# Kernel optimization log

Hardware: AMD Instinct MI355X
Metric: run time of the kernel (lower is better)

## Reference

```python
import jax, jax.numpy as jnp
import numpy as np

B, S, H = 4, 2048, 16
HID = 2048
Q_LORA = 1536
KV_LORA = 512
D_NOPE, D_ROPE, D_V = 128, 64, 128
D_QK = D_NOPE + D_ROPE  # 192
THETA = 10000.0
EPS = 1e-6


def rms_norm(x, w):
    var = jnp.mean(jnp.square(x), axis=-1, keepdims=True)
    return x * jax.lax.rsqrt(var + EPS) * w


def rotate_half(x):
    x1, x2 = jnp.split(x, 2, axis=-1)
    return jnp.concatenate([-x2, x1], axis=-1)


def apply_rope(x, cos, sin):
    # DeepSeek de-interleaves pairs before the rotate_half formulation
    b, h, s, d = x.shape
    x = x.reshape(b, h, s, d // 2, 2).transpose(0, 1, 2, 4, 3).reshape(b, h, s, d)
    return x * cos + rotate_half(x) * sin


def setup_inputs() -> dict:
    key = jax.random.key(0)
    ks = jax.random.split(key, 8)
    sc = lambda fan_in: 1.0 / np.sqrt(fan_in)
    return {
        "x": jax.random.normal(ks[0], (B, S, HID), jnp.float32),
        "q_a_w": jax.random.normal(ks[1], (Q_LORA, HID), jnp.float32) * sc(HID),
        "q_a_ln_w": jnp.ones((Q_LORA,), jnp.float32),
        "q_b_w": jax.random.normal(ks[2], (H * D_QK, Q_LORA), jnp.float32) * sc(Q_LORA),
        "kv_a_w": jax.random.normal(ks[3], (KV_LORA + D_ROPE, HID), jnp.float32) * sc(HID),
        "kv_a_ln_w": jnp.ones((KV_LORA,), jnp.float32),
        "kv_b_w": jax.random.normal(ks[4], (H * (D_NOPE + D_V), KV_LORA), jnp.float32) * sc(KV_LORA),
        "o_w": jax.random.normal(ks[5], (HID, H * D_V), jnp.float32) * sc(H * D_V),
    }


def reference(x, q_a_w, q_a_ln_w, q_b_w, kv_a_w, kv_a_ln_w, kv_b_w, o_w):
    b, s, _ = x.shape
    # --- Q path: low-rank down-proj -> RMSNorm -> up-proj ---
    q = rms_norm(x @ q_a_w.T, q_a_ln_w) @ q_b_w.T          # [b,s,H*D_QK]
    q = q.reshape(b, s, H, D_QK).transpose(0, 2, 1, 3)      # [b,H,s,D_QK]
    q_nope, q_pe = q[..., :D_NOPE], q[..., D_NOPE:]
    # --- KV path: joint low-rank compression + shared rope key ---
    ckv = x @ kv_a_w.T                                      # [b,s,KV_LORA+D_ROPE]
    c_kv, k_pe = ckv[..., :KV_LORA], ckv[..., KV_LORA:]
    k_pe = k_pe.reshape(b, 1, s, D_ROPE)                    # shared across heads (MQA-style)
    kv = rms_norm(c_kv, kv_a_ln_w) @ kv_b_w.T               # [b,s,H*(D_NOPE+D_V)]
    kv = kv.reshape(b, s, H, D_NOPE + D_V).transpose(0, 2, 1, 3)
    k_nope, v = kv[..., :D_NOPE], kv[..., D_NOPE:]
    # --- decoupled RoPE on the rope sub-dims ---
    inv_freq = 1.0 / (THETA ** (jnp.arange(0, D_ROPE, 2, dtype=jnp.float32) / D_ROPE))
    t = jnp.arange(s, dtype=jnp.float32)
    emb = jnp.concatenate([jnp.outer(t, inv_freq)] * 2, axis=-1)  # [s,D_ROPE]
    cos, sin = jnp.cos(emb)[None, None], jnp.sin(emb)[None, None]
    q_pe = apply_rope(q_pe, cos, sin)
    k_pe = apply_rope(k_pe, cos, sin)
    # --- attention (wrapper's all-True mask => unmasked softmax) ---
    q_full = jnp.concatenate([q_nope, q_pe], axis=-1)                       # [b,H,s,192]
    k_full = jnp.concatenate([k_nope, jnp.broadcast_to(k_pe, (b, H, s, D_ROPE))], axis=-1)
    scale = D_QK ** -0.5
    scores = jnp.einsum('bhqd,bhkd->bhqk', q_full, k_full) * scale
    attn = jax.nn.softmax(scores, axis=-1)
    out = jnp.einsum('bhqk,bhkd->bhqd', attn, v)
    out = out.transpose(0, 2, 1, 3).reshape(b, s, H * D_V)
    return out @ o_w.T
```

## Files before the change

kernel.cpp:

```cpp
#include <hip/hip_runtime.h>
#include <hip/hip_bf16.h>
#include <cstdint>
#include <cstddef>

typedef unsigned short u16;
typedef unsigned int   u32;

typedef __bf16 bf16x8 __attribute__((ext_vector_type(8)));
typedef float  f32x4  __attribute__((ext_vector_type(4)));
typedef float  f32x16 __attribute__((ext_vector_type(16)));
typedef u16    u16x4  __attribute__((ext_vector_type(4)));
typedef u16    u16x8  __attribute__((ext_vector_type(8)));
typedef u32    u32x4  __attribute__((ext_vector_type(4)));

#define DEV static __device__ __forceinline__
#define VMCNT(n) asm volatile("s_waitcnt vmcnt(" #n ")" ::: "memory")
#define LGKM0    asm volatile("s_waitcnt lgkmcnt(0)" ::: "memory")
#define SBARF    do { asm volatile("" ::: "memory"); __builtin_amdgcn_s_barrier(); asm volatile("" ::: "memory"); } while (0)

DEV u16 f2bf(float f){
  union { float f; u32 u; } v; v.f = f;
  u32 r = v.u + 0x7fffu + ((v.u >> 16) & 1u);
  return (u16)(r >> 16);
}
DEV float bf2f(u16 h){
  union { u32 u; float f; } v; v.u = ((u32)h) << 16;
  return v.f;
}
DEV u32 pk2(float a, float b){
  __hip_bfloat16 x = __float2bfloat16(a), y = __float2bfloat16(b);
  return (u32)__builtin_bit_cast(u16, x) | ((u32)__builtin_bit_cast(u16, y) << 16);
}
DEV float fexp2(float x){ float r; asm("v_exp_f32 %0, %1" : "=v"(r) : "v"(x)); return r; }
DEV float mx3(float a, float b, float c){ return fmaxf(fmaxf(a, b), c); }
DEV float tree16(const f32x16& p){
  float a = mx3(p[0],p[1],p[2]),  b = mx3(p[3],p[4],p[5]);
  float c = mx3(p[6],p[7],p[8]),  d = mx3(p[9],p[10],p[11]);
  float e = mx3(p[12],p[13],p[14]);
  return fmaxf(mx3(a,b,c), mx3(d,e,p[15]));
}
DEV void gll16(const void* g, void* l){
  __builtin_amdgcn_global_load_lds(
      (const __attribute__((address_space(1))) u32*)g,
      (__attribute__((address_space(3))) u32*)l, 16, 0, 0);
}

__global__ void k_cvt_all(const float* __restrict__ x,  const float* __restrict__ qaw,
                          const float* __restrict__ kvaw, const float* __restrict__ qbw,
                          const float* __restrict__ kvbw, const float* __restrict__ ow,
                          u16* __restrict__ xb, u16* __restrict__ w1, u16* __restrict__ wqb,
                          u16* __restrict__ wkvb, u16* __restrict__ wo,
                          float* __restrict__ tab){
  const long stride = (long)gridDim.x * blockDim.x;
  for (long i = (long)blockIdx.x * blockDim.x + threadIdx.x; i < 8192000L; i += stride){
    if (i >= 8126464L){
      int idx = (int)(i - 8126464L);
      int s = idx >> 5, p = idx & 31;
      float freq = exp2f(-(float)p * 0.41524101186f);
      float ang = (float)s * freq;
      tab[idx*2]   = cosf(ang);
      tab[idx*2+1] = sinf(ang);
      continue;
    }
    const float* src; u16* dst;
    if (i < 4194304L){ long e = i*4; src = x + e; dst = xb + e; }
    else if (i < 5373952L){
      long e = (i - 4194304L) * 4;
      int row = (int)(e >> 11), col = (int)(e & 2047);
      dst = w1 + e;
      if (row < 1536) src = qaw + (long)row*2048 + col;
      else if (row < 2048) src = kvaw + (long)(row-1536)*2048 + col;
      else if (row < 2112){
        int j = row - 2048;
        int sj = (j < 32) ? (2*j) : (2*(j-32)+1);
        src = kvaw + (long)(512 + sj)*2048 + col;
      }
      else { u16x4 z; z[0]=0;z[1]=0;z[2]=0;z[3]=0; *(u16x4*)dst = z; continue; }
    }
    else if (i < 6553600L){
      long e = (i - 5373952L)*4;
      int row = (int)(e / 1536), col = (int)(e - (long)row*1536);
      int dd = row % 192;
      int srow = row;
      if (dd >= 128){
        int j = dd - 128;
        int sdd = (j < 32) ? (128 + 2*j) : (128 + 2*(j - 32) + 1);
        srow = row - dd + sdd;
      }
      src = qbw + (long)srow*1536 + col; dst = wqb + e;
    }
    else if (i < 7077888L){ long e = (i - 6553600L)*4; src = kvbw + e; dst = wkvb + e; }
    else { long e = (i - 7077888L)*4; src = ow + e; dst = wo + e; }
    f32x4 f = *(const f32x4*)src;
    u16x4 o4;
    o4[0]=f2bf(f[0]); o4[1]=f2bf(f[1]); o4[2]=f2bf(f[2]); o4[3]=f2bf(f[3]);
    *(u16x4*)dst = o4;
  }
}

template<int CMODE>
DEV void gemm_body(u16 (*sm)[32768], int bm, int bn,
                   const u16* __restrict__ A, int lda,
                   const u16* __restrict__ B, int ldb,
                   void* __restrict__ Cp, int ldc, int K, int Nlim,
                   u16* __restrict__ kn, u16* __restrict__ vt,
                   const float* __restrict__ tab)
{
  const int tid = threadIdx.x;
  const int l   = tid & 63;
  const int wv  = tid >> 6;
  const int wr  = wv >> 2, wc = wv & 3;
  const int l15 = l & 15, l4 = l >> 4;
  const long M0 = (long)bm * 256, N0 = (long)bn * 256;

  const int c7 = tid & 7;
  const u16* asrc[4]; const u16* bsrc[4];
  int dsta[4], dstb[4];
  #pragma unroll
  for (int s = 0; s < 4; ++s){
    int slot = s*512 + tid;
    int row  = slot >> 3;
    asrc[s] = A + (M0 + row)*lda + ((c7 ^ (row & 7)) << 3);
    bsrc[s] = B + (N0 + row)*ldb + ((c7 ^ (row & 7)) << 3);
    dsta[s] = slot*8;
    dstb[s] = 16384 + slot*8;
  }
  auto stA = [&](int s, int kt, int nb){ gll16(asrc[s] + (long)kt*64, &sm[nb][dsta[s]]); };
  auto stB = [&](int s, int kt, int nb){ gll16(bsrc[s] + (long)kt*64, &sm[nb][dstb[s]]); };

  auto rdA = [&](int buf, int m, int ks) -> bf16x8 {
    int row = wr*128 + m*16 + l15;
    int ch  = ks*4 + l4;
    return *(const bf16x8*)&sm[buf][row*64 + ((ch ^ (row & 7)) << 3)];
  };
  auto rdB = [&](int buf, int n, int ks) -> bf16x8 {
    int row = wc*64 + n*16 + l15;
    int ch  = ks*4 + l4;
    return *(const bf16x8*)&sm[buf][16384 + row*64 + ((ch ^ (row & 7)) << 3)];
  };

  f32x4 acc[8][4];
  #pragma unroll
  for (int m = 0; m < 8; ++m)
    #pragma unroll
    for (int n = 0; n < 4; ++n)
      acc[m][n] = (f32x4)0.0f;

  stB(0,0,0); stB(2,0,0); stB(1,0,0); stB(3,0,0);
  stA(0,0,0); stA(2,0,0); stA(1,0,0); stA(3,0,0);
  VMCNT(2);
  SBARF;

  const int NT = K >> 6;
  for (int t = 0; t < NT; ++t){
    const int cb = t & 1, nb = cb ^ 1;
    const bool PF = (t + 1 < NT);
    bf16x8 bfr[4][2];
    #pragma unroll
    for (int p = 0; p < 4; ++p){
      bf16x8 af[2][2];
      #pragma unroll
      for (int mm = 0; mm < 2; ++mm)
        #pragma unroll
        for (int ks = 0; ks < 2; ++ks)
          af[mm][ks] = rdA(cb, p*2 + mm, ks);
      if (p == 0){
        #pragma unroll
        for (int n = 0; n < 4; ++n)
          #pragma unroll
          for (int ks = 0; ks < 2; ++ks)
            bfr[n][ks] = rdB(cb, n, ks);
        if (PF){ stB(0, t+1, nb); stB(2, t+1, nb); }
      } else if (p == 1){
        if (PF){ stB(1, t+1, nb); stB(3, t+1, nb); }
      } else if (p == 2){
        if (PF){ stA(0, t+1, nb); stA(2, t+1, nb); }
      } else {
        if (PF){ stA(1, t+1, nb); stA(3, t+1, nb); }
      }
      SBARF;
      LGKM0;
      __builtin_amdgcn_s_setprio(1);
      #pragma unroll
      for (int mm = 0; mm < 2; ++mm)
        #pragma unroll
        for (int n = 0; n < 4; ++n)
          #pragma unroll
          for (int ks = 0; ks < 2; ++ks)
            acc[p*2+mm][n] = __builtin_amdgcn_mfma_f32_16x16x32_bf16(af[mm][ks], bfr[n][ks], acc[p*2+mm][n], 0, 0, 0);
      __builtin_amdgcn_s_setprio(0);
      if (p == 1){ if (PF) VMCNT(4); else VMCNT(0); }
      if (p == 3 && PF) VMCNT(2);
      SBARF;
    }
  }

  const long rbase = M0 + wr*128 + l4*4;
  const long cbase = N0 + wc*64 + l15;

  if (CMODE == 3){
    const bool ropeblk = (((N0 + wc*64) % 192) == 128);
    if (ropeblk){
      #pragma unroll
      for (int n = 0; n < 2; ++n){
        const int p = l15 + 16*n;
        #pragma unroll
        for (int m = 0; m < 8; ++m){
          #pragma unroll
          for (int i = 0; i < 4; ++i){
            long r = rbase + m*16 + i;
            const float* cs2 = tab + (((int)(r & 2047))*32 + p)*2;
            float cs = cs2[0], sn = cs2[1];
            float e = acc[m][n][i], o = acc[m][n+2][i];
            ((u16*)Cp)[r * ldc + cbase + n*16]       = f2bf(e*cs - o*sn);
            ((u16*)Cp)[r * ldc + cbase + (n+2)*16]   = f2bf(o*cs + e*sn);
          }
        }
      }
    } else {
      #pragma unroll
      for (int m = 0; m < 8; ++m)
        #pragma unroll
        for (int n = 0; n < 4; ++n)
          #pragma unroll
          for (int i = 0; i < 4; ++i)
            ((u16*)Cp)[(rbase + m*16 + i) * ldc + cbase + n*16] = f2bf(acc[m][n][i]);
    }
    return;
  }

  #pragma unroll
  for (int m = 0; m < 8; ++m){
    #pragma unroll
    for (int n = 0; n < 4; ++n){
      const long c  = cbase + n*16;
      const long r0 = rbase + m*16;
      if (CMODE == 0){
        if (c < Nlim){
          #pragma unroll
          for (int i = 0; i < 4; ++i)
            ((u16*)Cp)[(r0 + i) * ldc + c] = f2bf(acc[m][n][i]);
        }
      } else if (CMODE == 1){
        #pragma unroll
        for (int i = 0; i < 4; ++i)
          ((float*)Cp)[(r0 + i) * ldc + c] = acc[m][n][i];
      } else {
        int h = (int)(c >> 8), rem = (int)(c & 255);
        if (rem < 128){
          #pragma unroll
          for (int i = 0; i < 4; ++i)
            kn[(r0 + i) * 2048 + h*128 + rem] = f2bf(acc[m][n][i]);
        } else {
          int bb = (int)(r0 >> 11), s = (int)(r0 & 2047);
          int kk = s & 63;
          int kkp = (kk & ~12) | ((kk & 4) << 1) | ((kk & 8) >> 1);
          int kt = s >> 6;
          int dfull = rem - 128;
          int bh = bb*16 + h;
          long idx = ((((long)bh*32 + kt)*4 + (dfull>>5))*8 + (kkp>>3))*256
                   + (dfull & 31)*8 + (kkp & 7);
          u16x4 pv;
          #pragma unroll
          for (int i = 0; i < 4; ++i) pv[i] = f2bf(acc[m][n][i]);
          *(u16x4*)&vt[idx] = pv;
        }
      }
    }
  }
}

template<int CMODE>
__global__ __launch_bounds__(512, 1)
void k_gemm8(const u16* __restrict__ A, int lda,
             const u16* __restrict__ B, int ldb,
             void* __restrict__ Cp, int ldc, int K, int Nlim, int gy,
             u16* __restrict__ kn, u16* __restrict__ vt)
{
  __shared__ u16 sm[2][32768];
  const int flat = blockIdx.x;
  const int id2  = (flat & 7) * ((int)gridDim.x >> 3) + (flat >> 3);
  gemm_body<CMODE>(sm, id2 / gy, id2 % gy, A, lda, B, ldb, Cp, ldc, K, Nlim, kn, vt, nullptr);
}

__global__ __launch_bounds__(512, 1)
void k_gemm_qbkvb(const u16* __restrict__ qackv, const u16* __restrict__ wqb,
                  const u16* __restrict__ wkvb, u16* __restrict__ q,
                  u16* __restrict__ kn, u16* __restrict__ vt,
                  const float* __restrict__ tab)
{
  __shared__ u16 sm[2][32768];
  const int flat = blockIdx.x;
  const int grp = flat >> 3, sub = flat & 7;
  if (grp < 48){
    int i = sub*48 + grp;
    gemm_body<3>(sm, i/12, i%12, qackv, 2176, wqb, 1536, q, 3072, 1536, 3072, nullptr, nullptr, tab);
  } else {
    int i = sub*64 + (grp - 48);
    gemm_body<2>(sm, i/16, i%16, qackv + 1536, 2176, wkvb, 512, nullptr, 0, 512, 4096, kn, vt, nullptr);
  }
}

__global__ __launch_bounds__(64)
void k_kpe(const u16* __restrict__ xb, const u16* __restrict__ w1,
           u16* __restrict__ qackv, const float* __restrict__ tab)
{
  const int l = threadIdx.x;
  const int l15 = l & 15, l4 = l >> 4;
  const long M0 = (long)blockIdx.x * 16;

  f32x4 acc[4];
  #pragma unroll
  for (int n = 0; n < 4; ++n) acc[n] = (f32x4)0.0f;

  const u16* aptr = xb + (M0 + l15)*2048 + l4*8;
  const u16* bptr = w1 + (2048 + l15)*2048 + l4*8;

  #pragma unroll 2
  for (int kt = 0; kt < 32; ++kt){
    bf16x8 a[2], b[4][2];
    #pragma unroll
    for (int ks = 0; ks < 2; ++ks)
      a[ks] = *(const bf16x8*)(aptr + kt*64 + ks*32);
    #pragma unroll
    for (int n = 0; n < 4; ++n)
      #pragma unroll
      for (int ks = 0; ks < 2; ++ks)
        b[n][ks] = *(const bf16x8*)(bptr + (long)n*16*2048 + kt*64 + ks*32);
    #pragma unroll
    for (int n = 0; n < 4; ++n)
      #pragma unroll
      for (int ks = 0; ks < 2; ++ks)
        acc[n] = __builtin_amdgcn_mfma_f32_16x16x32_bf16(a[ks], b[n][ks], acc[n], 0, 0, 0);
  }

  #pragma unroll
  for (int n = 0; n < 2; ++n){
    const int p = l15 + 16*n;
    #pragma unroll
    for (int i = 0; i < 4; ++i){
      long r = M0 + l4*4 + i;
      const float* cs2 = tab + (((int)(r & 2047))*32 + p)*2;
      float cs = cs2[0], sn = cs2[1];
      float e = acc[n][i], o = acc[n+2][i];
      qackv[r*2176 + 2048 + p]      = f2bf(e*cs - o*sn);
      qackv[r*2176 + 2048 + 32 + p] = f2bf(o*cs + e*sn);
    }
  }
}

__global__ __launch_bounds__(256)
void k_normrope(u16* __restrict__ qackv, const float* __restrict__ qln,
                const float* __restrict__ kvln){
  const int tok = blockIdx.x;
  const int tid = threadIdx.x;
  u16* row = qackv + (long)tok * 2176;
  __shared__ float red[8];

  float v[6]; float ss = 0.f;
  #pragma unroll
  for (int i = 0; i < 6; ++i){
    int c = tid + i*256;
    v[i] = bf2f(row[c]);
    ss += v[i]*v[i];
  }
  #pragma unroll
  for (int m = 32; m >= 1; m >>= 1) ss += __shfl_xor(ss, m);
  if ((tid & 63) == 0) red[tid >> 6] = ss;
  __syncthreads();
  float tot = red[0] + red[1] + red[2] + red[3];
  float r1 = rsqrtf(tot * (1.0f/1536.0f) + 1e-6f);
  #pragma unroll
  for (int i = 0; i < 6; ++i){
    int c = tid + i*256;
    row[c] = f2bf(v[i] * r1 * qln[c]);
  }

  float u0 = bf2f(row[1536 + tid]);
  float u1 = bf2f(row[1536 + 256 + tid]);
  float s2 = u0*u0 + u1*u1;
  #pragma unroll
  for (int m = 32; m >= 1; m >>= 1) s2 += __shfl_xor(s2, m);
  if ((tid & 63) == 0) red[4 + (tid >> 6)] = s2;
  __syncthreads();
  float tot2 = red[4] + red[5] + red[6] + red[7];
  float r2 = rsqrtf(tot2 * (1.0f/512.0f) + 1e-6f);
  row[1536 + tid]       = f2bf(u0 * r2 * kvln[tid]);
  row[1536 + 256 + tid] = f2bf(u1 * r2 * kvln[256 + tid]);
}

__global__ __launch_bounds__(512)
void k_attn11(const u16* __restrict__ Q, const u16* __restrict__ KN,
              const u16* __restrict__ CKV, const u16* __restrict__ VT,
              u16* __restrict__ O)
{
  __shared__ u16 sK[2][64*192];

  const int tid = threadIdx.x;
  const int l   = tid & 63;
  const int w   = tid >> 6;
  const int l31 = l & 31;
  const int hi  = l >> 5;
  const int swz = l31 & 7;
  const int flat = blockIdx.x;
  const int qb  = flat >> 6;
  const int bh  = ((flat & 7) << 3) | ((flat >> 3) & 7);
  const int b   = bh >> 4, h = bh & 15;
  const long tokbase = (long)b << 11;

  bf16x8 qf[12];
  {
    const u16* qptr = Q + (tokbase + qb*256 + w*32 + l31)*3072 + h*192 + hi*8;
    #pragma unroll
    for (int s = 0; s < 12; ++s)
      qf[s] = *(const bf16x8*)(qptr + s*16);
  }

  const u16* ksrc[3]; int kstep[3]; int kdst[3];
  #pragma unroll
  for (int i = 0; i < 3; ++i){
    int ch = tid + i*512;
    int row = ch / 24;
    int cc  = ch - row*24;
    int sc  = cc ^ (row & 7);
    if (sc < 16){ ksrc[i] = KN  + (tokbase + row)*2048 + h*128 + sc*8;       kstep[i] = 64*2048; }
    else        { ksrc[i] = CKV + (tokbase + row)*2176 + 2048 + (sc-16)*8;   kstep[i] = 64*2176; }
    kdst[i] = ch*8;
  }
  auto STAGE = [&](int kt, int nb){
    #pragma unroll
    for (int i = 0; i < 3; ++i) gll16(ksrc[i] + (long)kt*kstep[i], &sK[nb][kdst[i]]);
  };

  const u16* vbase = VT + (long)bh*(32*8192) + hi*256 + l31*8;

  f32x16 oacc[4];
  #pragma unroll
  for (int i = 0; i < 4; ++i) oacc[i] = (f32x16)0.0f;
  float mrun = -1e30f, lrun = 0.f;
  const float scale2 = (float)(0.07216878364870323 * 1.4426950408889634);

  STAGE(0, 0);
  __syncthreads();

  for (int kt = 0; kt < 32; ++kt){
    const int cur = kt & 1;
    if (kt < 31) STAGE(kt + 1, cur ^ 1);

    const char* kb = (const char*)&sK[cur][0];
    const u16*  vp = vbase + (long)kt*8192;

    f32x16 p0 = (f32x16)0.0f, p1 = (f32x16)0.0f;
    __builtin_amdgcn_s_setprio(1);
    #pragma unroll
    for (int s = 0; s < 12; ++s){
      const int co = ((2*s + hi) ^ swz) << 4;
      bf16x8 k0 = *(const bf16x8*)(kb + l31*384 + co);
      bf16x8 k1 = *(const bf16x8*)(kb + (32 + l31)*384 + co);
      p0 = __builtin_amdgcn_mfma_f32_32x32x16_bf16(k0, qf[s], p0, 0, 0, 0);
      p1 = __builtin_amdgcn_mfma_f32_32x32x16_bf16(k1, qf[s], p1, 0, 0, 0);
    }
    __builtin_amdgcn_s_setprio(0);

    bf16x8 vA0 = *(const bf16x8*)(vp + 0);
    bf16x8 vA1 = *(const bf16x8*)(vp + 2048);
    bf16x8 vA2 = *(const bf16x8*)(vp + 4096);
    bf16x8 vA3 = *(const bf16x8*)(vp + 6144);
    bf16x8 vB0 = *(const bf16x8*)(vp + 512);
    bf16x8 vB1 = *(const bf16x8*)(vp + 2560);
    bf16x8 vB2 = *(const bf16x8*)(vp + 4608);
    bf16x8 vB3 = *(const bf16x8*)(vp + 6656);

    float rm = fmaxf(tree16(p0), tree16(p1));
    rm = fmaxf(rm, __shfl_xor(rm, 32));
    const float om = rm * scale2;
    if (!__all(om <= mrun + 8.0f)){
      float mn = fmaxf(mrun, om);
      float corr = fexp2(mrun - mn);
      mrun = mn;
      lrun *= corr;
      #pragma unroll
      for (int d = 0; d < 4; ++d)
        #pragma unroll
        for (int r = 0; r < 16; ++r) oacc[d][r] *= corr;
    }
    float ls = 0.f;
    #pragma unroll
    for (int r = 0; r < 16; ++r){ p0[r] = fexp2(__builtin_fmaf(p0[r], scale2, -mrun)); ls += p0[r]; }
    #pragma unroll
    for (int r = 0; r < 16; ++r){ p1[r] = fexp2(__builtin_fmaf(p1[r], scale2, -mrun)); ls += p1[r]; }
    lrun += ls + __shfl_xor(ls, 32);

    bf16x8 pa[4];
    #pragma unroll
    for (int ks = 0; ks < 4; ++ks){
      const f32x16 ps = (ks < 2) ? p0 : p1;
      const int rb = (ks & 1) * 8;
      u32x4 aw;
      aw[0] = pk2(ps[rb+0], ps[rb+1]);
      aw[1] = pk2(ps[rb+2], ps[rb+3]);
      aw[2] = pk2(ps[rb+4], ps[rb+5]);
      aw[3] = pk2(ps[rb+6], ps[rb+7]);
      pa[ks] = __builtin_bit_cast(bf16x8, aw);
    }
    __builtin_amdgcn_s_setprio(1);
    bf16x8 vC0 = *(const bf16x8*)(vp + 1024);
    bf16x8 vC1 = *(const bf16x8*)(vp + 3072);
    bf16x8 vC2 = *(const bf16x8*)(vp + 5120);
    bf16x8 vC3 = *(const bf16x8*)(vp + 7168);
    oacc[0] = __builtin_amdgcn_mfma_f32_32x32x16_bf16(vA0, pa[0], oacc[0], 0, 0, 0);
    oacc[1] = __builtin_amdgcn_mfma_f32_32x32x16_bf16(vA1, pa[0], oacc[1], 0, 0, 0);
    oacc[2] = __builtin_amdgcn_mfma_f32_32x32x16_bf16(vA2, pa[0], oacc[2], 0, 0, 0);
    oacc[3] = __builtin_amdgcn_mfma_f32_32x32x16_bf16(vA3, pa[0], oacc[3], 0, 0, 0);
    bf16x8 vD0 = *(const bf16x8*)(vp + 1536);
    bf16x8 vD1 = *(const bf16x8*)(vp + 3584);
    bf16x8 vD2 = *(const bf16x8*)(vp + 5632);
    bf16x8 vD3 = *(const bf16x8*)(vp + 7680);
    oacc[0] = __builtin_amdgcn_mfma_f32_32x32x16_bf16(vB0, pa[1], oacc[0], 0, 0, 0);
    oacc[1] = __builtin_amdgcn_mfma_f32_32x32x16_bf16(vB1, pa[1], oacc[1], 0, 0, 0);
    oacc[2] = __builtin_amdgcn_mfma_f32_32x32x16_bf16(vB2, pa[1], oacc[2], 0, 0, 0);
    oacc[3] = __builtin_amdgcn_mfma_f32_32x32x16_bf16(vB3, pa[1], oacc[3], 0, 0, 0);
    oacc[0] = __builtin_amdgcn_mfma_f32_32x32x16_bf16(vC0, pa[2], oacc[0], 0, 0, 0);
    oacc[1] = __builtin_amdgcn_mfma_f32_32x32x16_bf16(vC1, pa[2], oacc[1], 0, 0, 0);
    oacc[2] = __builtin_amdgcn_mfma_f32_32x32x16_bf16(vC2, pa[2], oacc[2], 0, 0, 0);
    oacc[3] = __builtin_amdgcn_mfma_f32_32x32x16_bf16(vC3, pa[2], oacc[3], 0, 0, 0);
    oacc[0] = __builtin_amdgcn_mfma_f32_32x32x16_bf16(vD0, pa[3], oacc[0], 0, 0, 0);
    oacc[1] = __builtin_amdgcn_mfma_f32_32x32x16_bf16(vD1, pa[3], oacc[1], 0, 0, 0);
    oacc[2] = __builtin_amdgcn_mfma_f32_32x32x16_bf16(vD2, pa[3], oacc[2], 0, 0, 0);
    oacc[3] = __builtin_amdgcn_mfma_f32_32x32x16_bf16(vD3, pa[3], oacc[3], 0, 0, 0);
    __builtin_amdgcn_s_setprio(0);

    __syncthreads();
  }

  const float inv = 1.0f / lrun;
  u16* optr = O + (tokbase + qb*256 + w*32 + l31)*2048 + h*128;
  #pragma unroll
  for (int d = 0; d < 4; ++d){
    #pragma unroll
    for (int t = 0; t < 4; ++t){
      u16x4 ov;
      #pragma unroll
      for (int j = 0; j < 4; ++j) ov[j] = f2bf(oacc[d][4*t + j] * inv);
      *(u16x4*)(optr + d*32 + 8*t + 4*hi) = ov;
    }
  }
}

extern "C" void kernel_launch(void* const* d_in, const int* in_sizes, int n_in,
                              void* d_out, int out_size, void* d_ws, size_t ws_size,
                              hipStream_t stream)
{
  const float* x    = (const float*)d_in[0];
  const float* qaw  = (const float*)d_in[1];
  const float* qln  = (const float*)d_in[2];
  const float* qbw  = (const float*)d_in[3];
  const float* kvaw = (const float*)d_in[4];
  const float* kvln = (const float*)d_in[5];
  const float* kvbw = (const float*)d_in[6];
  const float* ow   = (const float*)d_in[7];

  char* ws = (char*)d_ws;
  size_t off = 0;
  auto alloc = [&](size_t bytes) -> void* {
    void* p = ws + off;
    off += (bytes + 255) & ~(size_t)255;
    return p;
  };
  u16* xb    = (u16*)alloc(8192UL*2048*2);
  u16* w1    = (u16*)alloc(2304UL*2048*2);
  u16* wqb   = (u16*)alloc(3072UL*1536*2);
  u16* wkvb  = (u16*)alloc(4096UL*512*2);
  u16* wo    = (u16*)alloc(2048UL*2048*2);
  u16* qackv = (u16*)alloc(8192UL*2176*2);
  u16* q     = (u16*)alloc(8192UL*3072*2);
  u16* kn    = (u16*)alloc(8192UL*2048*2);
  u16* vt    = (u16*)alloc(8192UL*2048*2);
  float* tab = (float*)alloc(2048UL*32*2*4);
  u16* ao    = xb;

  k_cvt_all<<<dim3(2048), dim3(256), 0, stream>>>(x, qaw, kvaw, qbw, kvbw, ow,
                                                  xb, w1, wqb, wkvb, wo, tab);
  k_gemm8<0><<<dim3(256), dim3(512), 0, stream>>>(xb, 2048, w1, 2048,
                                                  qackv, 2176, 2048, 2176, 8, nullptr, nullptr);
  k_kpe<<<dim3(512), dim3(64), 0, stream>>>(xb, w1, qackv, tab);
  k_normrope<<<dim3(8192), dim3(256), 0, stream>>>(qackv, qln, kvln);
  k_gemm_qbkvb<<<dim3(896), dim3(512), 0, stream>>>(qackv, wqb, wkvb, q, kn, vt, tab);
  k_attn11<<<dim3(512), dim3(512), 0, stream>>>(q, kn, qackv, vt, ao);
  k_gemm8<1><<<dim3(256), dim3(512), 0, stream>>>(ao, 2048, wo, 2048,
                                                  d_out, 2048, 2048, 2048, 8, nullptr, nullptr);
}
```

Before: 503.8 us.

## Fold k_pe projection into Q/KV up-proj launch and vectorize norm kernel

Removes the separate k_kpe launch by appending 64 extra blocks to the fused q_b/kv_b GEMM kernel. Each extra block runs eight waves, and each wave computes the rope-key projection and RoPE for 16 tokens. The RMSNorm kernel now loads and stores with 16-byte and 4-byte vectors and uses one barrier instead of two. This saves a launch and overlaps the small GEMM with the big one. The extra blocks write qackv columns 2048+ while other blocks read columns below that, and the 1-block-per-CU launch bound still applies to these light blocks.

```diff
diff --git a/kernel.cpp b/kernel.cpp
--- a/kernel.cpp
+++ b/kernel.cpp
@@ -287,10 +287,58 @@
 void k_gemm_qbkvb(const u16* __restrict__ qackv, const u16* __restrict__ wqb,
                   const u16* __restrict__ wkvb, u16* __restrict__ q,
                   u16* __restrict__ kn, u16* __restrict__ vt,
-                  const float* __restrict__ tab)
+                  const float* __restrict__ tab,
+                  const u16* __restrict__ xb, const u16* __restrict__ w1)
 {
   __shared__ u16 sm[2][32768];
   const int flat = blockIdx.x;
+  if (flat >= 896){
+    const int tid = threadIdx.x;
+    const int l   = tid & 63;
+    const int l15 = l & 15, l4 = l >> 4;
+    const int wvk = tid >> 6;
+    const long M0 = ((long)(flat - 896)*8 + wvk) * 16;
+
+    f32x4 acc[4];
+    #pragma unroll
+    for (int n = 0; n < 4; ++n) acc[n] = (f32x4)0.0f;
+
+    const u16* aptr = xb + (M0 + l15)*2048 + l4*8;
+    const u16* bptr = w1 + (2048 + l15)*2048 + l4*8;
+
+    #pragma unroll 2
+    for (int kt = 0; kt < 32; ++kt){
+      bf16x8 a[2], b[4][2];
+      #pragma unroll
+      for (int ks = 0; ks < 2; ++ks)
+        a[ks] = *(const bf16x8*)(aptr + kt*64 + ks*32);
+      #pragma unroll
+      for (int n = 0; n < 4; ++n)
+        #pragma unroll
+        for (int ks = 0; ks < 2; ++ks)
+          b[n][ks] = *(const bf16x8*)(bptr + (long)n*16*2048 + kt*64 + ks*32);
+      #pragma unroll
+      for (int n = 0; n < 4; ++n)
+        #pragma unroll
+        for (int ks = 0; ks < 2; ++ks)
+          acc[n] = __builtin_amdgcn_mfma_f32_16x16x32_bf16(a[ks], b[n][ks], acc[n], 0, 0, 0);
+    }
+
+    #pragma unroll
+    for (int n = 0; n < 2; ++n){
+      const int p = l15 + 16*n;
+      #pragma unroll
+      for (int i = 0; i < 4; ++i){
+        long r = M0 + l4*4 + i;
+        const float* cs2 = tab + (((int)(r & 2047))*32 + p)*2;
+        float cs = cs2[0], sn = cs2[1];
+        float e = acc[n][i], o = acc[n+2][i];
+        ((u16*)qackv)[r*2176 + 2048 + p]      = f2bf(e*cs - o*sn);
+        ((u16*)qackv)[r*2176 + 2048 + 32 + p] = f2bf(o*cs + e*sn);
+      }
+    }
+    return;
+  }
   const int grp = flat >> 3, sub = flat & 7;
   if (grp < 48){
     int i = sub*48 + grp;
@@ -301,54 +349,6 @@
   }
 }
 
-__global__ __launch_bounds__(64)
-void k_kpe(const u16* __restrict__ xb, const u16* __restrict__ w1,
-           u16* __restrict__ qackv, const float* __restrict__ tab)
-{
-  const int l = threadIdx.x;
-  const int l15 = l & 15, l4 = l >> 4;
-  const long M0 = (long)blockIdx.x * 16;
-
-  f32x4 acc[4];
-  #pragma unroll
-  for (int n = 0; n < 4; ++n) acc[n] = (f32x4)0.0f;
-
-  const u16* aptr = xb + (M0 + l15)*2048 + l4*8;
-  const u16* bptr = w1 + (2048 + l15)*2048 + l4*8;
-
-  #pragma unroll 2
-  for (int kt = 0; kt < 32; ++kt){
-    bf16x8 a[2], b[4][2];
-    #pragma unroll
-    for (int ks = 0; ks < 2; ++ks)
-      a[ks] = *(const bf16x8*)(aptr + kt*64 + ks*32);
-    #pragma unroll
-    for (int n = 0; n < 4; ++n)
-      #pragma unroll
-      for (int ks = 0; ks < 2; ++ks)
-        b[n][ks] = *(const bf16x8*)(bptr + (long)n*16*2048 + kt*64 + ks*32);
-    #pragma unroll
-    for (int n = 0; n < 4; ++n)
-      #pragma unroll
-      for (int ks = 0; ks < 2; ++ks)
-        acc[n] = __builtin_amdgcn_mfma_f32_16x16x32_bf16(a[ks], b[n][ks], acc[n], 0, 0, 0);
-  }
-
-  #pragma unroll
-  for (int n = 0; n < 2; ++n){
-    const int p = l15 + 16*n;
-    #pragma unroll
-    for (int i = 0; i < 4; ++i){
-      long r = M0 + l4*4 + i;
-      const float* cs2 = tab + (((int)(r & 2047))*32 + p)*2;
-      float cs = cs2[0], sn = cs2[1];
-      float e = acc[n][i], o = acc[n+2][i];
-      qackv[r*2176 + 2048 + p]      = f2bf(e*cs - o*sn);
-      qackv[r*2176 + 2048 + 32 + p] = f2bf(o*cs + e*sn);
-    }
-  }
-}
-
 __global__ __launch_bounds__(256)
 void k_normrope(u16* __restrict__ qackv, const float* __restrict__ qln,
                 const float* __restrict__ kvln){
@@ -357,36 +357,39 @@
   u16* row = qackv + (long)tok * 2176;
   __shared__ float red[8];
 
-  float v[6]; float ss = 0.f;
-  #pragma unroll
-  for (int i = 0; i < 6; ++i){
-    int c = tid + i*256;
-    v[i] = bf2f(row[c]);
-    ss += v[i]*v[i];
+  float v[8]; float ss = 0.f;
+  if (tid < 192){
+    u16x8 h8 = *(const u16x8*)(row + tid*8);
+    #pragma unroll
+    for (int i = 0; i < 8; ++i){ v[i] = bf2f(h8[i]); ss += v[i]*v[i]; }
   }
   #pragma unroll
   for (int m = 32; m >= 1; m >>= 1) ss += __shfl_xor(ss, m);
   if ((tid & 63) == 0) red[tid >> 6] = ss;
-  __syncthreads();
-  float tot = red[0] + red[1] + red[2] + red[3];
-  float r1 = rsqrtf(tot * (1.0f/1536.0f) + 1e-6f);
-  #pragma unroll
-  for (int i = 0; i < 6; ++i){
-    int c = tid + i*256;
-    row[c] = f2bf(v[i] * r1 * qln[c]);
-  }
-
-  float u0 = bf2f(row[1536 + tid]);
-  float u1 = bf2f(row[1536 + 256 + tid]);
+
+  u32 pair = *(const u32*)(row + 1536 + 2*tid);
+  float u0 = bf2f((u16)(pair & 0xffff));
+  float u1 = bf2f((u16)(pair >> 16));
   float s2 = u0*u0 + u1*u1;
   #pragma unroll
   for (int m = 32; m >= 1; m >>= 1) s2 += __shfl_xor(s2, m);
   if ((tid & 63) == 0) red[4 + (tid >> 6)] = s2;
   __syncthreads();
+
+  float tot = red[0] + red[1] + red[2] + red[3];
+  float r1 = rsqrtf(tot * (1.0f/1536.0f) + 1e-6f);
+  if (tid < 192){
+    u16x8 o8;
+    #pragma unroll
+    for (int i = 0; i < 8; ++i) o8[i] = f2bf(v[i] * r1 * qln[tid*8 + i]);
+    *(u16x8*)(row + tid*8) = o8;
+  }
+
   float tot2 = red[4] + red[5] + red[6] + red[7];
   float r2 = rsqrtf(tot2 * (1.0f/512.0f) + 1e-6f);
-  row[1536 + tid]       = f2bf(u0 * r2 * kvln[tid]);
-  row[1536 + 256 + tid] = f2bf(u1 * r2 * kvln[256 + tid]);
+  u16 w0 = f2bf(u0 * r2 * kvln[2*tid]);
+  u16 w1v = f2bf(u1 * r2 * kvln[2*tid + 1]);
+  *(u32*)(row + 1536 + 2*tid) = (u32)w0 | ((u32)w1v << 16);
 }
 
 __global__ __launch_bounds__(512)
@@ -583,9 +586,8 @@
                                                   xb, w1, wqb, wkvb, wo, tab);
   k_gemm8<0><<<dim3(256), dim3(512), 0, stream>>>(xb, 2048, w1, 2048,
                                                   qackv, 2176, 2048, 2176, 8, nullptr, nullptr);
-  k_kpe<<<dim3(512), dim3(64), 0, stream>>>(xb, w1, qackv, tab);
   k_normrope<<<dim3(8192), dim3(256), 0, stream>>>(qackv, qln, kvln);
-  k_gemm_qbkvb<<<dim3(896), dim3(512), 0, stream>>>(qackv, wqb, wkvb, q, kn, vt, tab);
+  k_gemm_qbkvb<<<dim3(960), dim3(512), 0, stream>>>(qackv, wqb, wkvb, q, kn, vt, tab, xb, w1);
   k_attn11<<<dim3(512), dim3(512), 0, stream>>>(q, kn, qackv, vt, ao);
   k_gemm8<1><<<dim3(256), dim3(512), 0, stream>>>(ao, 2048, wo, 2048,
                                                   d_out, 2048, 2048, 2048, 8, nullptr, nullptr);
```

After: 535.8 us. 6.4% more time.
